# Kernel tuning notes

Hardware: AMD Instinct MI355X
Metric: run time of the kernel (lower is better)

## Reference

```python
import jax, jax.numpy as jnp
import numpy as np

N, E, D = 50000, 500000, 128   # nodes, edges, input feature dim
H, F = 4, 32                    # num_heads, features_per_head (H*F == MLP output 128)


def _layer_norm(x, scale, bias, eps=1e-6):
    mu = jnp.mean(x, axis=-1, keepdims=True)
    var = jnp.var(x, axis=-1, keepdims=True)
    return (x - mu) * jax.lax.rsqrt(var + eps) * scale + bias


def setup_inputs() -> dict:
    key = jax.random.key(0)
    ks = jax.random.split(key, 6)
    s = lambda fan_in: 1.0 / np.sqrt(fan_in)
    return {
        "nodes": jax.random.normal(ks[0], (N, D), jnp.float32),
        "W1": jax.random.normal(ks[1], (D, 128), jnp.float32) * s(D),
        "b1": jnp.zeros((128,), jnp.float32),
        "ln1_scale": jnp.ones((128,), jnp.float32),
        "ln1_bias": jnp.zeros((128,), jnp.float32),
        "W2": jax.random.normal(ks[2], (128, H * F), jnp.float32) * s(128),
        "b2": jnp.zeros((H * F,), jnp.float32),
        "ln2_scale": jnp.ones((H * F,), jnp.float32),
        "ln2_bias": jnp.zeros((H * F,), jnp.float32),
        "senders": jax.random.randint(ks[3], (E,), 0, N, dtype=jnp.int32),
        "receivers": jax.random.randint(ks[4], (E,), 0, N, dtype=jnp.int32),
    }


def reference(nodes, W1, b1, ln1_scale, ln1_bias, W2, b2, ln2_scale, ln2_bias,
              senders, receivers):
    # attention_query MLP (MLPTorso: Dense -> LayerNorm -> relu, activate_final=True)
    h = jnp.maximum(_layer_norm(nodes @ W1 + b1, ln1_scale, ln1_bias), 0.0)
    h = jnp.maximum(_layer_norm(h @ W2 + b2, ln2_scale, ln2_bias), 0.0)
    q = h.reshape(N, H, F)                       # [N, H, F]

    # gather per-edge sender/receiver projections (same math as per-edge MLP)
    sent = q[senders]                            # [E, H, F]
    recv = q[receivers]                          # [E, H, F]

    # per-edge, per-head attention logits
    logits = jnp.einsum('ehf,ehf->eh', sent, recv) / jnp.sqrt(jnp.float32(F))

    # segment softmax over incoming edges of each receiver node (jraph semantics)
    seg_max = jax.ops.segment_max(logits, receivers, num_segments=N)
    seg_max = jnp.where(jnp.isfinite(seg_max), seg_max, 0.0)  # empty segments
    unnorm = jnp.exp(logits - seg_max[receivers])
    denom = jax.ops.segment_sum(unnorm, receivers, num_segments=N)
    weights = unnorm / denom[receivers]          # [E, H]

    # weighted messages, scatter-sum to receiver nodes
    messages = sent * weights[..., None]         # [E, H, F]
    agg = jax.ops.segment_sum(messages, receivers, num_segments=N)  # [N, H, F]

    # node update: activation then average over heads (avg_multi_head=True)
    out = jnp.maximum(agg, 0.0)
    return jnp.mean(out, axis=1)                 # [N, F]
```

## Files before the change

kernel.cpp:

```cpp
#include <hip/hip_runtime.h>

constexpr int D  = 128;
constexpr int NH = 4;
constexpr int NF = 32;

typedef __attribute__((ext_vector_type(8))) short bfrag;
typedef __attribute__((ext_vector_type(4))) float ffrag;

__device__ __forceinline__ unsigned short bf16h(float x) {
    unsigned u = __float_as_uint(x);
    u += 0x7fffu + ((u >> 16) & 1u);
    return (unsigned short)(u >> 16);
}
__device__ __forceinline__ float bf16tof(unsigned short h) {
    return __uint_as_float(((unsigned)h) << 16);
}

__device__ __forceinline__ void gload_lds16(const unsigned short* g, unsigned short* l)
{
    __builtin_amdgcn_global_load_lds(
        (const __attribute__((address_space(1))) void*)g,
        (__attribute__((address_space(3))) void*)l, 16, 0, 0);
}

__global__ __launch_bounds__(256) void prep_kernel(
    const float* __restrict__ W1, const float* __restrict__ W2,
    unsigned short* __restrict__ wt, int* __restrict__ cnt, int nz)
{
    if (blockIdx.x < 16) {
        const int L  = blockIdx.x >> 3;
        const int ct = blockIdx.x & 7;
        const float* W = L ? W2 : W1;
        const int ks   = threadIdx.x >> 6;
        const int lane = threadIdx.x & 63;
        const int lg = lane >> 4, lc = lane & 15;
        unsigned short* Hp = wt + ((size_t)(L * 2 + 0) * 32 + ct * 4 + ks) * 512 + lane * 8;
        unsigned short* Lp = wt + ((size_t)(L * 2 + 1) * 32 + ct * 4 + ks) * 512 + lane * 8;
        #pragma unroll
        for (int i = 0; i < 8; ++i) {
            const int k = ks * 32 + lg * 8 + i;
            const int c = ct * 16 + lc;
            const float v = W[(size_t)k * 128 + c];
            const unsigned short hh = bf16h(v);
            Hp[i] = hh;
            Lp[i] = bf16h(v - bf16tof(hh));
        }
    } else {
        const int i4 = ((blockIdx.x - 16) * 256 + threadIdx.x) * 4;
        if (i4 + 3 < nz) {
            *(int4*)&cnt[i4] = {0, 0, 0, 0};
        } else if (i4 < nz) {
            for (int i = i4; i < nz; ++i) cnt[i] = 0;
        }
    }
}

__global__ __launch_bounds__(256, 2) void mlp_hist_kernel(
    const float* __restrict__ X,
    const unsigned short* __restrict__ WF,
    const float* __restrict__ b1, const float* __restrict__ g1, const float* __restrict__ be1,
    const float* __restrict__ b2, const float* __restrict__ g2, const float* __restrict__ be2,
    unsigned short* __restrict__ Q, int N,
    const int* __restrict__ recv, int* __restrict__ cnt, int E, int mlpBlocks)
{
    __shared__ unsigned short Wlds[32768];

    if (blockIdx.x >= mlpBlocks) {
        const int tid0   = (blockIdx.x - mlpBlocks) * 256 + threadIdx.x;
        const int stride = (gridDim.x - mlpBlocks) * 256;
        for (int i = tid0; i < E; i += stride) atomicAdd(&cnt[recv[i]], 1);
        return;
    }

    constexpr int PW = 132;
    const int tid  = threadIdx.x;
    const int lane = tid & 63;
    const int wave = tid >> 6;
    const int lc   = lane & 15;
    const int lg   = lane >> 4;
    const int n0w  = blockIdx.x * 64 + wave * 16;

    bfrag ah[4], al[4];
    ffrag acc[8];

    {
        const int row = n0w + lc;
        const int rowx = (row < N) ? row : (N - 1);
        const float* xr = X + (size_t)rowx * 128 + lg * 8;
        #pragma unroll
        for (int ks = 0; ks < 4; ++ks) {
            const float4 a = *(const float4*)&xr[ks * 32];
            const float4 b = *(const float4*)&xr[ks * 32 + 4];
            const float f[8] = {a.x, a.y, a.z, a.w, b.x, b.y, b.z, b.w};
            #pragma unroll
            for (int i = 0; i < 8; ++i) {
                const unsigned short hh = bf16h(f[i]);
                ah[ks][i] = (short)hh;
                al[ks][i] = (short)bf16h(f[i] - bf16tof(hh));
            }
        }
    }

    float b1v[8], g1v[8], t1v[8], b2v[8], g2v[8], t2v[8];
    #pragma unroll
    for (int ct = 0; ct < 8; ++ct) {
        const int col = ct * 16 + lc;
        b1v[ct] = b1[col]; g1v[ct] = g1[col]; t1v[ct] = be1[col];
        b2v[ct] = b2[col]; g2v[ct] = g2[col]; t2v[ct] = be2[col];
    }

#define STAGE_LAYER(Lbase)                                                     \
    {                                                                          \
        _Pragma("unroll")                                                      \
        for (int i_ = 0; i_ < 16; ++i_) {                                      \
            const int ch_ = wave * 16 + i_;                                    \
            gload_lds16(WF + ((size_t)(Lbase) + ch_) * 512 + lane * 8,         \
                        &Wlds[ch_ * 512]);                                     \
        }                                                                      \
    }

#define GEMM_LDS()                                                             \
    _Pragma("unroll")                                                          \
    for (int ct_ = 0; ct_ < 8; ++ct_) {                                        \
        const unsigned short* bh_ = &Wlds[(ct_ * 4) * 512 + lane * 8];         \
        const unsigned short* bl_ = &Wlds[(32 + ct_ * 4) * 512 + lane * 8];    \
        ffrag aH_ = (ffrag){0.f,0.f,0.f,0.f}, aX_ = (ffrag){0.f,0.f,0.f,0.f};  \
        _Pragma("unroll")                                                      \
        for (int ks_ = 0; ks_ < 4; ++ks_) {                                    \
            const bfrag bh = *(const bfrag*)(bh_ + ks_ * 512);                 \
            const bfrag bl = *(const bfrag*)(bl_ + ks_ * 512);                 \
            aH_ = __builtin_amdgcn_mfma_f32_16x16x32_bf16(ah[ks_], bh, aH_, 0, 0, 0); \
            aX_ = __builtin_amdgcn_mfma_f32_16x16x32_bf16(ah[ks_], bl, aX_, 0, 0, 0); \
            aX_ = __builtin_amdgcn_mfma_f32_16x16x32_bf16(al[ks_], bh, aX_, 0, 0, 0); \
        }                                                                      \
        acc[ct_] = aH_ + aX_;                                                  \
    }

    STAGE_LAYER(0)
    __syncthreads();

    GEMM_LDS()
    __syncthreads();

    unsigned* scr = (unsigned*)Wlds + wave * (16 * PW);
    #pragma unroll
    for (int j = 0; j < 4; ++j) {
        float t[8], s = 0.f, ss = 0.f;
        #pragma unroll
        for (int ct = 0; ct < 8; ++ct) {
            t[ct] = acc[ct][j] + b1v[ct];
            s += t[ct]; ss += t[ct] * t[ct];
        }
        #pragma unroll
        for (int off = 1; off <= 8; off <<= 1) {
            s  += __shfl_xor(s,  off, 16);
            ss += __shfl_xor(ss, off, 16);
        }
        const float mu   = s * (1.f / 128.f);
        const float var  = fmaxf(ss * (1.f / 128.f) - mu * mu, 0.f);
        const float rstd = rsqrtf(var + 1e-6f);
        const int row = lg * 4 + j;
        #pragma unroll
        for (int ct = 0; ct < 8; ++ct) {
            const float o = fmaxf((t[ct] - mu) * rstd * g1v[ct] + t1v[ct], 0.f);
            const unsigned short hh = bf16h(o);
            const unsigned short ll = bf16h(o - bf16tof(hh));
            scr[row * PW + ct * 16 + lc] = (unsigned)hh | ((unsigned)ll << 16);
        }
    }

    asm volatile("s_waitcnt lgkmcnt(0)" ::: "memory");
    __builtin_amdgcn_sched_barrier(0);

    #pragma unroll
    for (int ks = 0; ks < 4; ++ks) {
        const uint4 r0 = *(const uint4*)&scr[lc * PW + ks * 32 + lg * 8];
        const uint4 r1 = *(const uint4*)&scr[lc * PW + ks * 32 + lg * 8 + 4];
        const unsigned rr[8] = {r0.x, r0.y, r0.z, r0.w, r1.x, r1.y, r1.z, r1.w};
        #pragma unroll
        for (int i = 0; i < 8; ++i) {
            ah[ks][i] = (short)(rr[i] & 0xffffu);
            al[ks][i] = (short)(rr[i] >> 16);
        }
    }
    __syncthreads();

    STAGE_LAYER(64)
    __syncthreads();

    GEMM_LDS()

#undef GEMM_LDS
#undef STAGE_LAYER

    #pragma unroll
    for (int j = 0; j < 4; ++j) {
        float t[8], s = 0.f, ss = 0.f;
        #pragma unroll
        for (int ct = 0; ct < 8; ++ct) {
            t[ct] = acc[ct][j] + b2v[ct];
            s += t[ct]; ss += t[ct] * t[ct];
        }
        #pragma unroll
        for (int off = 1; off <= 8; off <<= 1) {
            s  += __shfl_xor(s,  off, 16);
            ss += __shfl_xor(ss, off, 16);
        }
        const float mu   = s * (1.f / 128.f);
        const float var  = fmaxf(ss * (1.f / 128.f) - mu * mu, 0.f);
        const float rstd = rsqrtf(var + 1e-6f);
        const int grow = n0w + lg * 4 + j;
        if (grow < N) {
            #pragma unroll
            for (int ct = 0; ct < 8; ++ct) {
                const float o = fmaxf((t[ct] - mu) * rstd * g2v[ct] + t2v[ct], 0.f);
                Q[(size_t)grow * 128 + ct * 16 + lc] = bf16h(o);
            }
        }
    }
}

__global__ __launch_bounds__(256) void scan_blocks_kernel(
    const int* __restrict__ cnt, int* __restrict__ rowptr,
    int* __restrict__ bsum, int N)
{
    __shared__ int lds[256];
    const int tid = threadIdx.x;
    const int base = blockIdx.x * 1024 + tid * 4;
    int v0 = (base + 0 < N) ? cnt[base + 0] : 0;
    int v1 = (base + 1 < N) ? cnt[base + 1] : 0;
    int v2 = (base + 2 < N) ? cnt[base + 2] : 0;
    int v3 = (base + 3 < N) ? cnt[base + 3] : 0;
    const int tsum = v0 + v1 + v2 + v3;
    lds[tid] = tsum;
    __syncthreads();
    for (int off = 1; off < 256; off <<= 1) {
        int t = (tid >= off) ? lds[tid - off] : 0;
        __syncthreads();
        lds[tid] += t;
        __syncthreads();
    }
    int run = lds[tid] - tsum;
    if (base + 0 < N) rowptr[base + 0] = run;
    run += v0;
    if (base + 1 < N) rowptr[base + 1] = run;
    run += v1;
    if (base + 2 < N) rowptr[base + 2] = run;
    run += v2;
    if (base + 3 < N) rowptr[base + 3] = run;
    if (tid == 255) bsum[blockIdx.x] = lds[255];
}

__global__ __launch_bounds__(256) void scan_top_kernel(int* bsum, int nb)
{
    __shared__ int lds[256];
    const int tid = threadIdx.x;
    int v = (tid < nb) ? bsum[tid] : 0;
    lds[tid] = v;
    __syncthreads();
    for (int off = 1; off < 256; off <<= 1) {
        int t = (tid >= off) ? lds[tid - off] : 0;
        __syncthreads();
        lds[tid] += t;
        __syncthreads();
    }
    if (tid < nb) bsum[tid] = lds[tid] - v;
}

__global__ __launch_bounds__(256) void scan_add_kernel(
    int* __restrict__ rowptr, int* __restrict__ cursor,
    const int* __restrict__ bsum, int N, int E)
{
    int i = blockIdx.x * blockDim.x + threadIdx.x;
    if (i < N) {
        int v = rowptr[i] + bsum[i >> 10];
        rowptr[i] = v;
        cursor[i] = v;
    }
    if (i == 0) rowptr[N] = E;
}

__global__ __launch_bounds__(256) void fill_kernel(
    const int* __restrict__ senders, const int* __restrict__ receivers,
    int* __restrict__ cursor, int* __restrict__ ssend, int E)
{
    int e = blockIdx.x * blockDim.x + threadIdx.x;
    if (e < E) {
        int r = receivers[e];
        int pos = atomicAdd(&cursor[r], 1);
        ssend[pos] = senders[e];
    }
}

__global__ __launch_bounds__(256) void node_attn_kernel(
    const unsigned short* __restrict__ q, const int* __restrict__ rowptr,
    const int* __restrict__ ssend, float* __restrict__ out, int N)
{
    const int lane = threadIdx.x & 63;
    const int hl   = lane & 31;
    const int half = lane >> 5;
    const int wid  = (blockIdx.x * blockDim.x + threadIdx.x) >> 6;
    const int nw   = (gridDim.x * blockDim.x) >> 6;

    for (int n = wid; n < N; n += nw) {
        const uint2 braw = *(const uint2*)&q[(size_t)n * D + hl * 4];
        const float b0 = __uint_as_float(braw.x << 16);
        const float b1 = __uint_as_float(braw.x & 0xffff0000u);
        const float b2 = __uint_as_float(braw.y << 16);
        const float b3 = __uint_as_float(braw.y & 0xffff0000u);

        const int beg = rowptr[n], end = rowptr[n + 1];
        float m = -1e30f, l = 0.f;
        float c0 = 0.f, c1 = 0.f, c2 = 0.f, c3 = 0.f;

        int j = beg + half;
        uint2 raw = {0u, 0u};
        if (j < end)
            raw = *(const uint2*)&q[(size_t)ssend[j] * D + hl * 4];
        for (; j < end; j += 2) {
            const uint2 cur = raw;
            if (j + 2 < end)
                raw = *(const uint2*)&q[(size_t)ssend[j + 2] * D + hl * 4];
            const float a0 = __uint_as_float(cur.x << 16);
            const float a1 = __uint_as_float(cur.x & 0xffff0000u);
            const float a2 = __uint_as_float(cur.y << 16);
            const float a3 = __uint_as_float(cur.y & 0xffff0000u);
            float p = a0 * b0 + a1 * b1 + a2 * b2 + a3 * b3;
            p += __shfl_xor(p, 1);
            p += __shfl_xor(p, 2);
            p += __shfl_xor(p, 4);
            const float logit = p * 0.17677669529663687f;
            const float nm = fmaxf(m, logit);
            const float sc = __expf(m - nm);
            const float u  = __expf(logit - nm);
            l  = l * sc + u;
            c0 = c0 * sc + u * a0;
            c1 = c1 * sc + u * a1;
            c2 = c2 * sc + u * a2;
            c3 = c3 * sc + u * a3;
            m = nm;
        }

        const float om  = __shfl_xor(m, 32);
        const float ol  = __shfl_xor(l, 32);
        const float oc0 = __shfl_xor(c0, 32);
        const float oc1 = __shfl_xor(c1, 32);
        const float oc2 = __shfl_xor(c2, 32);
        const float oc3 = __shfl_xor(c3, 32);
        const float nm = fmaxf(m, om);
        const float s0 = __expf(m - nm), s1 = __expf(om - nm);
        const float lt = l * s0 + ol * s1;
        const float inv = (lt > 0.f) ? (1.f / lt) : 0.f;
        float r0 = fmaxf((c0 * s0 + oc0 * s1) * inv, 0.f);
        float r1 = fmaxf((c1 * s0 + oc1 * s1) * inv, 0.f);
        float r2 = fmaxf((c2 * s0 + oc2 * s1) * inv, 0.f);
        float r3 = fmaxf((c3 * s0 + oc3 * s1) * inv, 0.f);

        r0 += __shfl_xor(r0, 8);  r0 += __shfl_xor(r0, 16);
        r1 += __shfl_xor(r1, 8);  r1 += __shfl_xor(r1, 16);
        r2 += __shfl_xor(r2, 8);  r2 += __shfl_xor(r2, 16);
        r3 += __shfl_xor(r3, 8);  r3 += __shfl_xor(r3, 16);
        if (lane < 8) {
            float4 o = {0.25f * r0, 0.25f * r1, 0.25f * r2, 0.25f * r3};
            *(float4*)&out[(size_t)n * NF + lane * 4] = o;
        }
    }
}

extern "C" void kernel_launch(void* const* d_in, const int* in_sizes, int n_in,
                              void* d_out, int out_size, void* d_ws, size_t ws_size,
                              hipStream_t stream)
{
    const float* nodes = (const float*)d_in[0];
    const float* W1    = (const float*)d_in[1];
    const float* b1    = (const float*)d_in[2];
    const float* g1    = (const float*)d_in[3];
    const float* be1   = (const float*)d_in[4];
    const float* W2    = (const float*)d_in[5];
    const float* b2    = (const float*)d_in[6];
    const float* g2    = (const float*)d_in[7];
    const float* be2   = (const float*)d_in[8];
    const int* senders   = (const int*)d_in[9];
    const int* receivers = (const int*)d_in[10];

    const int N = in_sizes[0] / D;
    const int E = in_sizes[9];
    float* out = (float*)d_out;

    char* ws = (char*)d_ws;
    unsigned short* qb = (unsigned short*)ws; ws += (size_t)N * D * 2;
    unsigned short* wt = (unsigned short*)ws; ws += 4 * 128 * 128 * 2;
    int* cnt      = (int*)ws;    ws += (size_t)N * 4;
    int* rowptr   = (int*)ws;    ws += (size_t)(N + 2) * 4;
    int* cursor   = (int*)ws;    ws += (size_t)N * 4;
    int* bsum     = (int*)ws;    ws += 256 * 4;
    int* ssend    = (int*)ws;    ws += (size_t)E * 4;

    const int zb = (N + 1023) / 1024;
    const int mlpBlocks = (N + 63) / 64;
    const int nb = (N + 1023) / 1024;

    prep_kernel<<<16 + zb, 256, 0, stream>>>(W1, W2, wt, cnt, N);

    mlp_hist_kernel<<<mlpBlocks + 128, 256, 0, stream>>>(
        nodes, wt, b1, g1, be1, b2, g2, be2, qb, N,
        receivers, cnt, E, mlpBlocks);

    scan_blocks_kernel<<<nb, 256, 0, stream>>>(cnt, rowptr, bsum, N);
    scan_top_kernel<<<1, 256, 0, stream>>>(bsum, nb);
    scan_add_kernel<<<(N + 255) / 256, 256, 0, stream>>>(rowptr, cursor, bsum, N, E);

    fill_kernel<<<(E + 255) / 256, 256, 0, stream>>>(senders, receivers, cursor, ssend, E);

    node_attn_kernel<<<(N + 3) / 4, 256, 0, stream>>>(qb, rowptr, ssend, out, N);
}
```

Measured before the change: 119.1 us.

## Read MLP weight fragments straight from global memory instead of staging in LDS

The MLP kernel stops staging each layer's 64 KB bf16 hi/lo weight fragments into LDS with block barriers. Each wave now loads the B fragments directly from global memory, which should be served from L2 since every block reads the same data. LDS use drops to a small per-wave scratch for the layer-1 activations, so the occupancy hint rises from 2 to 4 blocks per CU and the block-wide syncs go away. The cost is more global/L2 traffic per wave and possible load latency stalls in front of the MFMAs.

```diff
diff --git a/kernel.cpp b/kernel.cpp
--- a/kernel.cpp
+++ b/kernel.cpp
@@ -14,13 +14,6 @@
 }
 __device__ __forceinline__ float bf16tof(unsigned short h) {
     return __uint_as_float(((unsigned)h) << 16);
-}
-
-__device__ __forceinline__ void gload_lds16(const unsigned short* g, unsigned short* l)
-{
-    __builtin_amdgcn_global_load_lds(
-        (const __attribute__((address_space(1))) void*)g,
-        (__attribute__((address_space(3))) void*)l, 16, 0, 0);
 }
 
 __global__ __launch_bounds__(256) void prep_kernel(
@@ -55,7 +48,7 @@
     }
 }
 
-__global__ __launch_bounds__(256, 2) void mlp_hist_kernel(
+__global__ __launch_bounds__(256, 4) void mlp_hist_kernel(
     const float* __restrict__ X,
     const unsigned short* __restrict__ WF,
     const float* __restrict__ b1, const float* __restrict__ g1, const float* __restrict__ be1,
@@ -63,7 +56,8 @@
     unsigned short* __restrict__ Q, int N,
     const int* __restrict__ recv, int* __restrict__ cnt, int E, int mlpBlocks)
 {
-    __shared__ unsigned short Wlds[32768];
+    constexpr int PW = 132;
+    __shared__ unsigned HL[4 * 16 * PW];
 
     if (blockIdx.x >= mlpBlocks) {
         const int tid0   = (blockIdx.x - mlpBlocks) * 256 + threadIdx.x;
@@ -72,20 +66,20 @@
         return;
     }
 
-    constexpr int PW = 132;
     const int tid  = threadIdx.x;
     const int lane = tid & 63;
     const int wave = tid >> 6;
     const int lc   = lane & 15;
     const int lg   = lane >> 4;
-    const int n0w  = blockIdx.x * 64 + wave * 16;
+    const int n0w  = (blockIdx.x * 4 + wave) * 16;
+    if (n0w >= N) return;
+    unsigned* hl = &HL[wave * 16 * PW];
 
     bfrag ah[4], al[4];
     ffrag acc[8];
 
     {
-        const int row = n0w + lc;
-        const int rowx = (row < N) ? row : (N - 1);
+        const int rowx = (n0w + lc < N) ? (n0w + lc) : (N - 1);
         const float* xr = X + (size_t)rowx * 128 + lg * 8;
         #pragma unroll
         for (int ks = 0; ks < 4; ++ks) {
@@ -101,6 +95,25 @@
         }
     }
 
+    auto gemm = [&](int hiBase, int loBase) {
+        #pragma unroll
+        for (int ct = 0; ct < 8; ++ct) {
+            const unsigned short* bhp = WF + (size_t)(hiBase + ct * 4) * 512 + lane * 8;
+            const unsigned short* blp = WF + (size_t)(loBase + ct * 4) * 512 + lane * 8;
+            ffrag a = (ffrag){0.f, 0.f, 0.f, 0.f};
+            ffrag x = (ffrag){0.f, 0.f, 0.f, 0.f};
+            #pragma unroll
+            for (int ks = 0; ks < 4; ++ks) {
+                const bfrag bh = *(const bfrag*)(bhp + ks * 512);
+                const bfrag bl = *(const bfrag*)(blp + ks * 512);
+                a = __builtin_amdgcn_mfma_f32_16x16x32_bf16(ah[ks], bh, a, 0, 0, 0);
+                x = __builtin_amdgcn_mfma_f32_16x16x32_bf16(ah[ks], bl, x, 0, 0, 0);
+                x = __builtin_amdgcn_mfma_f32_16x16x32_bf16(al[ks], bh, x, 0, 0, 0);
+            }
+            acc[ct] = a + x;
+        }
+    };
+
     float b1v[8], g1v[8], t1v[8], b2v[8], g2v[8], t2v[8];
     #pragma unroll
     for (int ct = 0; ct < 8; ++ct) {
@@ -109,40 +122,8 @@
         b2v[ct] = b2[col]; g2v[ct] = g2[col]; t2v[ct] = be2[col];
     }
 
-#define STAGE_LAYER(Lbase)                                                     \
-    {                                                                          \
-        _Pragma("unroll")                                                      \
-        for (int i_ = 0; i_ < 16; ++i_) {                                      \
-            const int ch_ = wave * 16 + i_;                                    \
-            gload_lds16(WF + ((size_t)(Lbase) + ch_) * 512 + lane * 8,         \
-                        &Wlds[ch_ * 512]);                                     \
-        }                                                                      \
-    }
-
-#define GEMM_LDS()                                                             \
-    _Pragma("unroll")                                                          \
-    for (int ct_ = 0; ct_ < 8; ++ct_) {                                        \
-        const unsigned short* bh_ = &Wlds[(ct_ * 4) * 512 + lane * 8];         \
-        const unsigned short* bl_ = &Wlds[(32 + ct_ * 4) * 512 + lane * 8];    \
-        ffrag aH_ = (ffrag){0.f,0.f,0.f,0.f}, aX_ = (ffrag){0.f,0.f,0.f,0.f};  \
-        _Pragma("unroll")                                                      \
-        for (int ks_ = 0; ks_ < 4; ++ks_) {                                    \
-            const bfrag bh = *(const bfrag*)(bh_ + ks_ * 512);                 \
-            const bfrag bl = *(const bfrag*)(bl_ + ks_ * 512);                 \
-            aH_ = __builtin_amdgcn_mfma_f32_16x16x32_bf16(ah[ks_], bh, aH_, 0, 0, 0); \
-            aX_ = __builtin_amdgcn_mfma_f32_16x16x32_bf16(ah[ks_], bl, aX_, 0, 0, 0); \
-            aX_ = __builtin_amdgcn_mfma_f32_16x16x32_bf16(al[ks_], bh, aX_, 0, 0, 0); \
-        }                                                                      \
-        acc[ct_] = aH_ + aX_;                                                  \
-    }
-
-    STAGE_LAYER(0)
-    __syncthreads();
-
-    GEMM_LDS()
-    __syncthreads();
-
-    unsigned* scr = (unsigned*)Wlds + wave * (16 * PW);
+    gemm(0, 32);
+
     #pragma unroll
     for (int j = 0; j < 4; ++j) {
         float t[8], s = 0.f, ss = 0.f;
@@ -165,7 +146,7 @@
             const float o = fmaxf((t[ct] - mu) * rstd * g1v[ct] + t1v[ct], 0.f);
             const unsigned short hh = bf16h(o);
             const unsigned short ll = bf16h(o - bf16tof(hh));
-            scr[row * PW + ct * 16 + lc] = (unsigned)hh | ((unsigned)ll << 16);
+            hl[row * PW + ct * 16 + lc] = (unsigned)hh | ((unsigned)ll << 16);
         }
     }
 
@@ -174,8 +155,8 @@
 
     #pragma unroll
     for (int ks = 0; ks < 4; ++ks) {
-        const uint4 r0 = *(const uint4*)&scr[lc * PW + ks * 32 + lg * 8];
-        const uint4 r1 = *(const uint4*)&scr[lc * PW + ks * 32 + lg * 8 + 4];
+        const uint4 r0 = *(const uint4*)&hl[lc * PW + ks * 32 + lg * 8];
+        const uint4 r1 = *(const uint4*)&hl[lc * PW + ks * 32 + lg * 8 + 4];
         const unsigned rr[8] = {r0.x, r0.y, r0.z, r0.w, r1.x, r1.y, r1.z, r1.w};
         #pragma unroll
         for (int i = 0; i < 8; ++i) {
@@ -183,15 +164,8 @@
             al[ks][i] = (short)(rr[i] >> 16);
         }
     }
-    __syncthreads();
-
-    STAGE_LAYER(64)
-    __syncthreads();
-
-    GEMM_LDS()
-
-#undef GEMM_LDS
-#undef STAGE_LAYER
+
+    gemm(64, 96);
 
     #pragma unroll
     for (int j = 0; j < 4; ++j) {
@@ -397,7 +371,8 @@
     int* ssend    = (int*)ws;    ws += (size_t)E * 4;
 
     const int zb = (N + 1023) / 1024;
-    const int mlpBlocks = (N + 63) / 64;
+    const int nwt = (N + 15) / 16;
+    const int mlpBlocks = (nwt + 3) / 4;
     const int nb = (N + 1023) / 1024;
 
     prep_kernel<<<16 + zb, 256, 0, stream>>>(W1, W2, wt, cnt, N);
```

Measured after the change: 124.8 us. +4.8%, slower.

## Halve MLP LDS footprint via K-half weight staging and dual-chain attention loop

Applied to the files above, without the earlier changes.

The MLP kernel now stages each layer's split bf16 weights in two K-halves through a 32 KB LDS buffer instead of 64 KB. It also raises the launch-bounds occupancy hint from 2 to 4 blocks and drops the scratch row padding. The three MFMAs now accumulate into a single chain instead of two. Separately, the node attention loop runs two independent online-softmax accumulators with two outstanding gathers per lane, merging them at the end. This aims to increase occupancy and memory-level parallelism, at the cost of extra barriers, possible LDS bank conflicts from removing the padding, and register pressure.

```diff
diff --git a/kernel.cpp b/kernel.cpp
--- a/kernel.cpp
+++ b/kernel.cpp
@@ -55,7 +55,7 @@
     }
 }
 
-__global__ __launch_bounds__(256, 2) void mlp_hist_kernel(
+__global__ __launch_bounds__(256, 4) void mlp_hist_kernel(
     const float* __restrict__ X,
     const unsigned short* __restrict__ WF,
     const float* __restrict__ b1, const float* __restrict__ g1, const float* __restrict__ be1,
@@ -63,7 +63,7 @@
     unsigned short* __restrict__ Q, int N,
     const int* __restrict__ recv, int* __restrict__ cnt, int E, int mlpBlocks)
 {
-    __shared__ unsigned short Wlds[32768];
+    __shared__ unsigned short Wlds[16384];
 
     if (blockIdx.x >= mlpBlocks) {
         const int tid0   = (blockIdx.x - mlpBlocks) * 256 + threadIdx.x;
@@ -72,7 +72,7 @@
         return;
     }
 
-    constexpr int PW = 132;
+    constexpr int PW = 128;
     const int tid  = threadIdx.x;
     const int lane = tid & 63;
     const int wave = tid >> 6;
@@ -109,37 +109,45 @@
         b2v[ct] = b2[col]; g2v[ct] = g2[col]; t2v[ct] = be2[col];
     }
 
-#define STAGE_LAYER(Lbase)                                                     \
+#define STAGE_KHALF(hiBase, loBase, h)                                         \
     {                                                                          \
         _Pragma("unroll")                                                      \
-        for (int i_ = 0; i_ < 16; ++i_) {                                      \
-            const int ch_ = wave * 16 + i_;                                    \
-            gload_lds16(WF + ((size_t)(Lbase) + ch_) * 512 + lane * 8,         \
-                        &Wlds[ch_ * 512]);                                     \
+        for (int i_ = 0; i_ < 8; ++i_) {                                       \
+            const int s_   = wave * 8 + i_;                                    \
+            const int p_   = s_ >> 4;                                          \
+            const int ct_  = (s_ & 15) >> 1;                                   \
+            const int ksl_ = s_ & 1;                                           \
+            const int chunk_ = (p_ ? (loBase) : (hiBase)) + ct_ * 4 + 2 * (h) + ksl_; \
+            gload_lds16(WF + (size_t)chunk_ * 512 + lane * 8, &Wlds[s_ * 512]);\
         }                                                                      \
     }
 
-#define GEMM_LDS()                                                             \
+#define GEMM_KHALF(h)                                                          \
     _Pragma("unroll")                                                          \
     for (int ct_ = 0; ct_ < 8; ++ct_) {                                        \
-        const unsigned short* bh_ = &Wlds[(ct_ * 4) * 512 + lane * 8];         \
-        const unsigned short* bl_ = &Wlds[(32 + ct_ * 4) * 512 + lane * 8];    \
-        ffrag aH_ = (ffrag){0.f,0.f,0.f,0.f}, aX_ = (ffrag){0.f,0.f,0.f,0.f};  \
+        ffrag a_ = acc[ct_];                                                   \
         _Pragma("unroll")                                                      \
-        for (int ks_ = 0; ks_ < 4; ++ks_) {                                    \
-            const bfrag bh = *(const bfrag*)(bh_ + ks_ * 512);                 \
-            const bfrag bl = *(const bfrag*)(bl_ + ks_ * 512);                 \
-            aH_ = __builtin_amdgcn_mfma_f32_16x16x32_bf16(ah[ks_], bh, aH_, 0, 0, 0); \
-            aX_ = __builtin_amdgcn_mfma_f32_16x16x32_bf16(ah[ks_], bl, aX_, 0, 0, 0); \
-            aX_ = __builtin_amdgcn_mfma_f32_16x16x32_bf16(al[ks_], bh, aX_, 0, 0, 0); \
+        for (int ksl_ = 0; ksl_ < 2; ++ksl_) {                                 \
+            const bfrag bh_ = *(const bfrag*)&Wlds[(ct_ * 2 + ksl_) * 512 + lane * 8];      \
+            const bfrag bl_ = *(const bfrag*)&Wlds[(16 + ct_ * 2 + ksl_) * 512 + lane * 8]; \
+            const int k_ = 2 * (h) + ksl_;                                     \
+            a_ = __builtin_amdgcn_mfma_f32_16x16x32_bf16(ah[k_], bh_, a_, 0, 0, 0); \
+            a_ = __builtin_amdgcn_mfma_f32_16x16x32_bf16(ah[k_], bl_, a_, 0, 0, 0); \
+            a_ = __builtin_amdgcn_mfma_f32_16x16x32_bf16(al[k_], bh_, a_, 0, 0, 0); \
         }                                                                      \
-        acc[ct_] = aH_ + aX_;                                                  \
-    }
-
-    STAGE_LAYER(0)
-    __syncthreads();
-
-    GEMM_LDS()
+        acc[ct_] = a_;                                                         \
+    }
+
+    #pragma unroll
+    for (int i = 0; i < 8; ++i) acc[i] = (ffrag){0.f, 0.f, 0.f, 0.f};
+
+    STAGE_KHALF(0, 32, 0)
+    __syncthreads();
+    GEMM_KHALF(0)
+    __syncthreads();
+    STAGE_KHALF(0, 32, 1)
+    __syncthreads();
+    GEMM_KHALF(1)
     __syncthreads();
 
     unsigned* scr = (unsigned*)Wlds + wave * (16 * PW);
@@ -185,13 +193,19 @@
     }
     __syncthreads();
 
-    STAGE_LAYER(64)
-    __syncthreads();
-
-    GEMM_LDS()
-
-#undef GEMM_LDS
-#undef STAGE_LAYER
+    #pragma unroll
+    for (int i = 0; i < 8; ++i) acc[i] = (ffrag){0.f, 0.f, 0.f, 0.f};
+
+    STAGE_KHALF(64, 96, 0)
+    __syncthreads();
+    GEMM_KHALF(0)
+    __syncthreads();
+    STAGE_KHALF(64, 96, 1)
+    __syncthreads();
+    GEMM_KHALF(1)
+
+#undef GEMM_KHALF
+#undef STAGE_KHALF
 
     #pragma unroll
     for (int j = 0; j < 4; ++j) {
@@ -310,21 +324,16 @@
         const float b3 = __uint_as_float(braw.y & 0xffff0000u);
 
         const int beg = rowptr[n], end = rowptr[n + 1];
-        float m = -1e30f, l = 0.f;
-        float c0 = 0.f, c1 = 0.f, c2 = 0.f, c3 = 0.f;
-
-        int j = beg + half;
-        uint2 raw = {0u, 0u};
-        if (j < end)
-            raw = *(const uint2*)&q[(size_t)ssend[j] * D + hl * 4];
-        for (; j < end; j += 2) {
-            const uint2 cur = raw;
-            if (j + 2 < end)
-                raw = *(const uint2*)&q[(size_t)ssend[j + 2] * D + hl * 4];
-            const float a0 = __uint_as_float(cur.x << 16);
-            const float a1 = __uint_as_float(cur.x & 0xffff0000u);
-            const float a2 = __uint_as_float(cur.y << 16);
-            const float a3 = __uint_as_float(cur.y & 0xffff0000u);
+
+        float mA = -1e30f, lA = 0.f, cA0 = 0.f, cA1 = 0.f, cA2 = 0.f, cA3 = 0.f;
+        float mB = -1e30f, lB = 0.f, cB0 = 0.f, cB1 = 0.f, cB2 = 0.f, cB3 = 0.f;
+
+        auto step = [&](uint2 c, float& m, float& l,
+                        float& s0r, float& s1r, float& s2r, float& s3r) {
+            const float a0 = __uint_as_float(c.x << 16);
+            const float a1 = __uint_as_float(c.x & 0xffff0000u);
+            const float a2 = __uint_as_float(c.y << 16);
+            const float a3 = __uint_as_float(c.y & 0xffff0000u);
             float p = a0 * b0 + a1 * b1 + a2 * b2 + a3 * b3;
             p += __shfl_xor(p, 1);
             p += __shfl_xor(p, 2);
@@ -333,28 +342,57 @@
             const float nm = fmaxf(m, logit);
             const float sc = __expf(m - nm);
             const float u  = __expf(logit - nm);
-            l  = l * sc + u;
-            c0 = c0 * sc + u * a0;
-            c1 = c1 * sc + u * a1;
-            c2 = c2 * sc + u * a2;
-            c3 = c3 * sc + u * a3;
+            l   = l   * sc + u;
+            s0r = s0r * sc + u * a0;
+            s1r = s1r * sc + u * a1;
+            s2r = s2r * sc + u * a2;
+            s3r = s3r * sc + u * a3;
             m = nm;
-        }
-
-        const float om  = __shfl_xor(m, 32);
-        const float ol  = __shfl_xor(l, 32);
-        const float oc0 = __shfl_xor(c0, 32);
-        const float oc1 = __shfl_xor(c1, 32);
-        const float oc2 = __shfl_xor(c2, 32);
-        const float oc3 = __shfl_xor(c3, 32);
-        const float nm = fmaxf(m, om);
-        const float s0 = __expf(m - nm), s1 = __expf(om - nm);
-        const float lt = l * s0 + ol * s1;
+        };
+
+        int jA = beg + half;
+        int jB = jA + 2;
+        uint2 rA = {0u, 0u}, rB = {0u, 0u};
+        if (jA < end) rA = *(const uint2*)&q[(size_t)ssend[jA] * D + hl * 4];
+        if (jB < end) rB = *(const uint2*)&q[(size_t)ssend[jB] * D + hl * 4];
+
+        for (; jB < end; jA += 4, jB += 4) {
+            const uint2 cA = rA, cB = rB;
+            if (jA + 4 < end)
+                rA = *(const uint2*)&q[(size_t)ssend[jA + 4] * D + hl * 4];
+            if (jB + 4 < end)
+                rB = *(const uint2*)&q[(size_t)ssend[jB + 4] * D + hl * 4];
+            step(cA, mA, lA, cA0, cA1, cA2, cA3);
+            step(cB, mB, lB, cB0, cB1, cB2, cB3);
+        }
+        if (jA < end)
+            step(rA, mA, lA, cA0, cA1, cA2, cA3);
+
+        {
+            const float nm = fmaxf(mA, mB);
+            const float s0 = __expf(mA - nm), s1 = __expf(mB - nm);
+            lA  = lA  * s0 + lB  * s1;
+            cA0 = cA0 * s0 + cB0 * s1;
+            cA1 = cA1 * s0 + cB1 * s1;
+            cA2 = cA2 * s0 + cB2 * s1;
+            cA3 = cA3 * s0 + cB3 * s1;
+            mA = nm;
+        }
+
+        const float om  = __shfl_xor(mA, 32);
+        const float ol  = __shfl_xor(lA, 32);
+        const float oc0 = __shfl_xor(cA0, 32);
+        const float oc1 = __shfl_xor(cA1, 32);
+        const float oc2 = __shfl_xor(cA2, 32);
+        const float oc3 = __shfl_xor(cA3, 32);
+        const float nm = fmaxf(mA, om);
+        const float s0 = __expf(mA - nm), s1 = __expf(om - nm);
+        const float lt = lA * s0 + ol * s1;
         const float inv = (lt > 0.f) ? (1.f / lt) : 0.f;
-        float r0 = fmaxf((c0 * s0 + oc0 * s1) * inv, 0.f);
-        float r1 = fmaxf((c1 * s0 + oc1 * s1) * inv, 0.f);
-        float r2 = fmaxf((c2 * s0 + oc2 * s1) * inv, 0.f);
-        float r3 = fmaxf((c3 * s0 + oc3 * s1) * inv, 0.f);
+        float r0 = fmaxf((cA0 * s0 + oc0 * s1) * inv, 0.f);
+        float r1 = fmaxf((cA1 * s0 + oc1 * s1) * inv, 0.f);
+        float r2 = fmaxf((cA2 * s0 + oc2 * s1) * inv, 0.f);
+        float r3 = fmaxf((cA3 * s0 + oc3 * s1) * inv, 0.f);
 
         r0 += __shfl_xor(r0, 8);  r0 += __shfl_xor(r0, 16);
         r1 += __shfl_xor(r1, 8);  r1 += __shfl_xor(r1, 16);
```

Measured after the change: 126.7 us. 1.06x slower.
